# Kernel tuning notes

Measured on AMD Instinct MI355X. Metric: run time of the kernel, lower is better.

Reference implementation:

```python
import jax, jax.numpy as jnp
import numpy as np

B, T, I, H, O = 64, 256, 256, 1024, 256


def _lstm_cell(x, h, c, W_ih, W_hh, b_ih, b_hh):
    # PyTorch LSTMCell: gates = x@W_ih^T + b_ih + h@W_hh^T + b_hh, chunked as i,f,g,o
    gates = x @ W_ih.T + h @ W_hh.T + (b_ih + b_hh)
    i_g, f_g, g_g, o_g = jnp.split(gates, 4, axis=-1)
    c_new = jax.nn.sigmoid(f_g) * c + jax.nn.sigmoid(i_g) * jnp.tanh(g_g)
    h_new = jax.nn.sigmoid(o_g) * jnp.tanh(c_new)
    return h_new, c_new


def setup_inputs() -> dict:
    key = jax.random.key(0)
    ks = jax.random.split(key, 11)
    s1 = 1.0 / np.sqrt(H)
    return {
        "x": jax.random.normal(ks[0], (B, T, I), dtype=jnp.float32),
        "W_ih1": jax.random.uniform(ks[1], (4 * H, I), jnp.float32, -s1, s1),
        "W_hh1": jax.random.uniform(ks[2], (4 * H, H), jnp.float32, -s1, s1),
        "b_ih1": jax.random.uniform(ks[3], (4 * H,), jnp.float32, -s1, s1),
        "b_hh1": jax.random.uniform(ks[4], (4 * H,), jnp.float32, -s1, s1),
        "W_ih2": jax.random.uniform(ks[5], (4 * H, I + H), jnp.float32, -s1, s1),
        "W_hh2": jax.random.uniform(ks[6], (4 * H, H), jnp.float32, -s1, s1),
        "b_ih2": jax.random.uniform(ks[7], (4 * H,), jnp.float32, -s1, s1),
        "b_hh2": jax.random.uniform(ks[8], (4 * H,), jnp.float32, -s1, s1),
        "W_l": jax.random.uniform(ks[9], (O, I + H), jnp.float32, -s1, s1),
        "b_l": jax.random.uniform(ks[10], (O,), jnp.float32, -s1, s1),
    }


def reference(x, W_ih1, W_hh1, b_ih1, b_hh1, W_ih2, W_hh2, b_ih2, b_hh2, W_l, b_l):
    batch = x.shape[0]
    zeros = jnp.zeros((batch, H), dtype=x.dtype)
    init = (zeros, zeros, zeros, zeros)  # h1, c1, h2, c2

    def step(carry, x_t):
        h1, c1, h2, c2 = carry
        h1, c1 = _lstm_cell(x_t, h1, c1, W_ih1, W_hh1, b_ih1, b_hh1)
        x2 = jnp.concatenate([x_t, h1], axis=1)  # [B, I+H]
        h2, c2 = _lstm_cell(x2, h2, c2, W_ih2, W_hh2, b_ih2, b_hh2)
        x3 = jnp.concatenate([x_t, h2], axis=1)  # [B, I+H]
        y_t = x3 @ W_l.T + b_l  # [B, O]
        return (h1, c1, h2, c2), y_t

    xs = jnp.swapaxes(x, 0, 1)  # [T, B, I]
    _, ys = jax.lax.scan(step, init, xs)  # ys: [T, B, O]
    return jnp.swapaxes(ys, 0, 1)  # [B, T, O]
```

## Files before the change

kernel.cpp:

```cpp
#include <hip/hip_runtime.h>


typedef __attribute__((ext_vector_type(8))) short short8;
typedef __attribute__((ext_vector_type(16))) float f32x16;
typedef __attribute__((ext_vector_type(4))) float f32x4;

#define Tn 256
#define In 256
#define Hn 1024
#define On 256
#define SP 136
#define NL1 64
#define NL2 128
#define NY  16
#define NBLK (NL1 + NL2 + NY)
#define CHUNK_B 17408
#define SMEM_SZ 55808
#define BHe 65536
#define RELEASE_IDX 240

#define WS_WIH1 0
#define WS_WHH1 2097152
#define WS_WIH2 10485760
#define WS_WHH2 20971520
#define WS_WL   29360128
#define WS_X    30015488
#define WS_H1   38404096
#define WS_H2   38666240
#define WS_ARR  38928384

#define WAIT_LGKM0() __builtin_amdgcn_s_waitcnt(0xC07F)
#define RAW_BARRIER() do { \
    WAIT_LGKM0(); \
    __builtin_amdgcn_sched_barrier(0); \
    __builtin_amdgcn_s_barrier(); \
    __builtin_amdgcn_sched_barrier(0); \
  } while (0)

#define STAGE_WAIT(rem) do { \
    __builtin_amdgcn_sched_barrier(0); \
    if ((rem) >= 3)      asm volatile("s_waitcnt vmcnt(12)" ::: "memory"); \
    else if ((rem) == 2) asm volatile("s_waitcnt vmcnt(8)"  ::: "memory"); \
    else if ((rem) == 1) asm volatile("s_waitcnt vmcnt(4)"  ::: "memory"); \
    else                 asm volatile("s_waitcnt vmcnt(0)"  ::: "memory"); \
    __builtin_amdgcn_sched_barrier(0); \
  } while (0)

#define GLD16(dst, ptr) \
  asm volatile("global_load_dwordx4 %0, %1, off" : "=v"(dst) : "v"(ptr))
#define GLD16C(dst, ptr) \
  asm volatile("global_load_dwordx4 %0, %1, off sc1" : "=v"(dst) : "v"(ptr))

static __device__ __forceinline__ unsigned short f2b(float f) {
  union { float f; unsigned int i; } v; v.f = f;
  unsigned int u = v.i;
  return (unsigned short)((u + 0x7FFFu + ((u >> 16) & 1u)) >> 16);
}
static __device__ __forceinline__ float sigm(float x) { return 1.0f / (1.0f + __expf(-x)); }
static __device__ __forceinline__ float tanhf_(float x) {
  float ax = fabsf(x);
  float e = __expf(-2.0f * ax);
  return copysignf((1.0f - e) / (1.0f + e), x);
}
static __device__ __forceinline__ int ld32a(const void* p) {
  return __hip_atomic_load((const int*)p, __ATOMIC_RELAXED, __HIP_MEMORY_SCOPE_AGENT);
}
static __device__ __forceinline__ void st32a(void* p, unsigned int v) {
  __hip_atomic_store((unsigned int*)p, v, __ATOMIC_RELAXED, __HIP_MEMORY_SCOPE_AGENT);
}
static __device__ __forceinline__ void st64a(void* p, unsigned long long v) {
  __hip_atomic_store((unsigned long long*)p, v, __ATOMIC_RELAXED, __HIP_MEMORY_SCOPE_AGENT);
}

static __device__ __forceinline__ void grid_barrier(int* arrive, int bid, int tid,
                                                    int lane, int tgt) {
  __syncthreads();
  if (tid == 0)
    st32a(&arrive[bid], (unsigned int)tgt);
  if (bid == 0) {
    if (tid < 64) {
      bool done = false;
      while (!done) {
        bool ok = true;
        #pragma unroll
        for (int j = 0; j < 4; ++j) {
          int idx = lane + j * 64;
          if (idx < NBLK) {
            int v = ld32a(&arrive[idx]);
            ok = ok && (v >= tgt);
          }
        }
        done = __all(ok);
        if (!done) __builtin_amdgcn_s_sleep(1);
      }
      if (tid == 0)
        st32a(&arrive[RELEASE_IDX], (unsigned int)tgt);
    }
    __syncthreads();
  } else {
    if (tid == 0) {
      while (ld32a(&arrive[RELEASE_IDX]) < tgt) __builtin_amdgcn_s_sleep(1);
    }
    __syncthreads();
  }
}

__global__ void __launch_bounds__(256) cvt_bf16(const float* __restrict__ src,
                                                unsigned short* __restrict__ dst, int n4) {
  int i = blockIdx.x * blockDim.x + threadIdx.x;
  if (i >= n4) return;
  float4 v = ((const float4*)src)[i];
  ushort4 o;
  o.x = f2b(v.x); o.y = f2b(v.y); o.z = f2b(v.z); o.w = f2b(v.w);
  ((ushort4*)dst)[i] = o;
}

__global__ void __launch_bounds__(256) prep_zero(unsigned short* h1buf,
                                                 unsigned short* h2buf,
                                                 int* arrive) {
  int i = blockIdx.x * blockDim.x + threadIdx.x;
  st64a((unsigned long long*)h1buf + i, 0ull);
  st64a((unsigned long long*)h1buf + 16384 + i, 0ull);
  st64a((unsigned long long*)h2buf + i, 0ull);
  st64a((unsigned long long*)h2buf + 16384 + i, 0ull);
  if (i < 256) st32a(arrive + i, 0u);
}

__global__ void __launch_bounds__(256, 1) lstm_persist(
    const unsigned short* __restrict__ x,
    const unsigned short* __restrict__ Wih1, const unsigned short* __restrict__ Whh1,
    const float* __restrict__ bih1, const float* __restrict__ bhh1,
    const unsigned short* __restrict__ Wih2, const unsigned short* __restrict__ Whh2,
    const float* __restrict__ bih2, const float* __restrict__ bhh2,
    const unsigned short* __restrict__ Wl,  const float* __restrict__ bl,
    float* __restrict__ out,
    unsigned short* __restrict__ h1buf, unsigned short* __restrict__ h2buf,
    int* __restrict__ arrive)
{
  extern __shared__ char smem[];
  unsigned short* sbuf0 = (unsigned short*)smem;
  unsigned short* sbuf1 = (unsigned short*)(smem + CHUNK_B);
  float* sG = (float*)(smem + 2 * CHUNK_B);
  float* sc = (float*)(smem + 2 * CHUNK_B + 16896);

  const int tid = threadIdx.x;
  const int bid = blockIdx.x;
  const int lane = tid & 63;
  const int wid = tid >> 6;
  const int r0  = tid >> 4;
  const int sg  = tid & 15;

  for (int e = tid; e < 1024; e += 256) sc[e] = 0.0f;

  uint4 rs[4][4];

  if (bid < NL1) {
    const int j0 = bid << 4;
    const int mtile = wid & 1, ntile = wid >> 1;
    const int arow = mtile * 32 + (lane & 31);
    const int brow = ntile * 32 + (lane & 31);
    const int gr = ((brow >> 4) << 10) + j0 + (brow & 15);
    const int hi8 = (lane >> 5) << 3;

    short8 w[80];
    #pragma unroll
    for (int c = 0; c < 10; ++c) {
      const unsigned short* wrow = (c < 2) ? (Wih1 + (size_t)gr * In + c * 128)
                                           : (Whh1 + (size_t)gr * Hn + (c - 2) * 128);
      #pragma unroll
      for (int k8 = 0; k8 < 8; ++k8)
        w[c * 8 + k8] = *(const short8*)(wrow + k8 * 16 + hi8);
    }
    float bs[2][2][4];
    #pragma unroll
    for (int p = 0; p < 2; ++p) {
      int pi = tid + p * 256, op = (pi & 7) << 1;
      #pragma unroll
      for (int k = 0; k < 2; ++k) {
        int o = op + k;
        #pragma unroll
        for (int g = 0; g < 4; ++g)
          bs[p][k][g] = bih1[g * 1024 + j0 + o] + bhh1[g * 1024 + j0 + o];
      }
    }

    for (int s = 0; s < Tn; ++s) {
      const int t = s;
      const unsigned short* h1rd = h1buf + ((t + 1) & 1) * BHe;
      unsigned short* h1wr = h1buf + (t & 1) * BHe;
      f32x16 acc0 = {}, acc1 = {};

      auto ldc = [&](int cc, int d) {
        if (cc < 2) {
          const char* p = (const char*)(x + ((size_t)r0 * Tn + t) * In + cc * 128 + sg * 8);
          #pragma unroll
          for (int j = 0; j < 4; ++j) GLD16(rs[d][j], p + (size_t)j * (16 * Tn * In * 2));
        } else {
          const char* p = (const char*)(h1rd + (size_t)r0 * Hn + (cc - 2) * 128 + sg * 8);
          #pragma unroll
          for (int j = 0; j < 4; ++j) GLD16C(rs[d][j], p + j * (16 * Hn * 2));
        }
      };
      ldc(0, 0); ldc(1, 1); ldc(2, 2); ldc(3, 3);

      #pragma unroll
      for (int c = 0; c < 10; ++c) {
        unsigned short* buf = (c & 1) ? sbuf1 : sbuf0;
        STAGE_WAIT(9 - c);
        {
          unsigned short* db = buf + r0 * SP + sg * 8;
          #pragma unroll
          for (int j = 0; j < 4; ++j) *(uint4*)(db + j * (16 * SP)) = rs[c & 3][j];
        }
        if (c + 4 < 10) ldc(c + 4, c & 3);
        RAW_BARRIER();
        const unsigned short* ab = buf + arow * SP + hi8;
        #pragma unroll
        for (int k8 = 0; k8 < 8; k8 += 2) {
          acc0 = __builtin_amdgcn_mfma_f32_32x32x16_bf16(*(const short8*)(ab + k8 * 16),      w[c * 8 + k8],     acc0, 0, 0, 0);
          acc1 = __builtin_amdgcn_mfma_f32_32x32x16_bf16(*(const short8*)(ab + k8 * 16 + 16), w[c * 8 + k8 + 1], acc1, 0, 0, 0);
        }
      }
      RAW_BARRIER();

      f32x16 accv = acc0 + acc1;
      #pragma unroll
      for (int i = 0; i < 16; ++i) {
        int rm = (i & 3) + ((i >> 2) << 3) + ((lane >> 5) << 2);
        sG[(mtile * 32 + rm) * 65 + brow] = accv[i];
      }
      __syncthreads();

      #pragma unroll
      for (int p = 0; p < 2; ++p) {
        int pi = tid + p * 256;
        int b = pi >> 3, op = (pi & 7) << 1;
        const float* gb = sG + b * 65;
        unsigned int pack = 0;
        #pragma unroll
        for (int k = 0; k < 2; ++k) {
          int o = op + k, e = b * 16 + o;
          float ig = gb[o]      + bs[p][k][0];
          float fg = gb[16 + o] + bs[p][k][1];
          float gg = gb[32 + o] + bs[p][k][2];
          float og = gb[48 + o] + bs[p][k][3];
          float cn = sigm(fg) * sc[e] + sigm(ig) * tanhf_(gg);
          sc[e] = cn;
          pack |= ((unsigned int)f2b(sigm(og) * tanhf_(cn))) << (16 * k);
        }
        st32a(h1wr + b * Hn + j0 + op, pack);
      }
      grid_barrier(arrive, bid, tid, lane, s + 1);
    }
    grid_barrier(arrive, bid, tid, lane, Tn + 1);

  } else if (bid < NL1 + NL2) {
    const int j0 = (bid - NL1) << 3;
    const int mtile = wid & 1, ks = wid >> 1;
    const int arow = mtile * 32 + (lane & 31);
    const int brow = lane & 31;
    const int gr = ((brow >> 3) << 10) + j0 + (brow & 7);
    const int hi8 = (lane >> 5) << 3;

    short8 w[80];
    if (ks == 0) {
      #pragma unroll
      for (int c = 0; c < 10; ++c)
        #pragma unroll
        for (int k8 = 0; k8 < 8; ++k8)
          w[c * 8 + k8] = *(const short8*)(Wih2 + (size_t)gr * 1280 + c * 128 + k8 * 16 + hi8);
    } else {
      #pragma unroll
      for (int c = 0; c < 8; ++c)
        #pragma unroll
        for (int k8 = 0; k8 < 8; ++k8)
          w[c * 8 + k8] = *(const short8*)(Whh2 + (size_t)gr * Hn + c * 128 + k8 * 16 + hi8);
    }
    float bs[2][4];
    {
      int op = (tid & 3) << 1;
      #pragma unroll
      for (int k = 0; k < 2; ++k) {
        int o = op + k;
        #pragma unroll
        for (int g = 0; g < 4; ++g)
          bs[k][g] = bih2[g * 1024 + j0 + o] + bhh2[g * 1024 + j0 + o];
      }
    }

    grid_barrier(arrive, bid, tid, lane, 1);

    for (int s = 1; s <= Tn; ++s) {
      const int t = s - 1;
      const unsigned short* h1rd = h1buf + (t & 1) * BHe;
      const unsigned short* h2rd = h2buf + ((t + 1) & 1) * BHe;
      unsigned short* h2wr = h2buf + (t & 1) * BHe;
      f32x16 acc0 = {}, acc1 = {};

      auto ldc = [&](int cc, int d) {
        if (cc < 2) {
          const char* p = (const char*)(x + ((size_t)r0 * Tn + t) * In + cc * 128 + sg * 8);
          #pragma unroll
          for (int j = 0; j < 4; ++j) GLD16(rs[d][j], p + (size_t)j * (16 * Tn * In * 2));
        } else {
          const unsigned short* src = (cc < 10) ? (h1rd + (cc - 2) * 128)
                                                : (h2rd + (cc - 10) * 128);
          const char* p = (const char*)(src + (size_t)r0 * Hn + sg * 8);
          #pragma unroll
          for (int j = 0; j < 4; ++j) GLD16C(rs[d][j], p + j * (16 * Hn * 2));
        }
      };
      ldc(0, 0); ldc(1, 1); ldc(2, 2); ldc(3, 3);

      #pragma unroll
      for (int c = 0; c < 18; ++c) {
        unsigned short* buf = (c & 1) ? sbuf1 : sbuf0;
        STAGE_WAIT(17 - c);
        {
          unsigned short* db = buf + r0 * SP + sg * 8;
          #pragma unroll
          for (int j = 0; j < 4; ++j) *(uint4*)(db + j * (16 * SP)) = rs[c & 3][j];
        }
        if (c + 4 < 18) ldc(c + 4, c & 3);
        RAW_BARRIER();
        bool active = (ks == 0) ? (c < 10) : (c >= 10);
        if (active) {
          int ib = ((ks == 0) ? c : (c - 10)) * 8;
          const unsigned short* ab = buf + arow * SP + hi8;
          #pragma unroll
          for (int k8 = 0; k8 < 8; k8 += 2) {
            acc0 = __builtin_amdgcn_mfma_f32_32x32x16_bf16(*(const short8*)(ab + k8 * 16),      w[ib + k8],     acc0, 0, 0, 0);
            acc1 = __builtin_amdgcn_mfma_f32_32x32x16_bf16(*(const short8*)(ab + k8 * 16 + 16), w[ib + k8 + 1], acc1, 0, 0, 0);
          }
        }
      }
      RAW_BARRIER();

      f32x16 accv = acc0 + acc1;
      #pragma unroll
      for (int i = 0; i < 16; ++i) {
        int rm = (i & 3) + ((i >> 2) << 3) + ((lane >> 5) << 2);
        sG[ks * 2112 + (mtile * 32 + rm) * 33 + brow] = accv[i];
      }
      __syncthreads();

      {
        int b = tid >> 2, op = (tid & 3) << 1;
        const float* g0 = sG + b * 33;
        const float* g1 = sG + 2112 + b * 33;
        unsigned int pack = 0;
        #pragma unroll
        for (int k = 0; k < 2; ++k) {
          int o = op + k, e = b * 8 + o;
          float ig = g0[o]      + g1[o]      + bs[k][0];
          float fg = g0[8 + o]  + g1[8 + o]  + bs[k][1];
          float gg = g0[16 + o] + g1[16 + o] + bs[k][2];
          float og = g0[24 + o] + g1[24 + o] + bs[k][3];
          float cn = sigm(fg) * sc[e] + sigm(ig) * tanhf_(gg);
          sc[e] = cn;
          pack |= ((unsigned int)f2b(sigm(og) * tanhf_(cn))) << (16 * k);
        }
        st32a(h2wr + b * Hn + j0 + op, pack);
      }
      grid_barrier(arrive, bid, tid, lane, s + 1);
    }

  } else {
    const int o0 = (bid - NL1 - NL2) << 4;
    const int quad = lane >> 4;
    const int l15 = lane & 15;
    const int hi8y = quad << 3;

    short8 wy[40];
    #pragma unroll
    for (int c = 0; c < 10; ++c)
      #pragma unroll
      for (int q = 0; q < 4; ++q)
        wy[c * 4 + q] = *(const short8*)(Wl + (size_t)(o0 + l15) * 1280 + c * 128 + q * 32 + hi8y);
    const float blv = bl[o0 + l15];

    grid_barrier(arrive, bid, tid, lane, 1);
    grid_barrier(arrive, bid, tid, lane, 2);

    for (int s = 2; s <= Tn + 1; ++s) {
      const int t = s - 2;
      const unsigned short* h2rd = h2buf + (t & 1) * BHe;
      f32x4 acc0 = {}, acc1 = {};

      auto ldc = [&](int cc, int d) {
        if (cc < 2) {
          const char* p = (const char*)(x + ((size_t)r0 * Tn + t) * In + cc * 128 + sg * 8);
          #pragma unroll
          for (int j = 0; j < 4; ++j) GLD16(rs[d][j], p + (size_t)j * (16 * Tn * In * 2));
        } else {
          const char* p = (const char*)(h2rd + (size_t)r0 * Hn + (cc - 2) * 128 + sg * 8);
          #pragma unroll
          for (int j = 0; j < 4; ++j) GLD16C(rs[d][j], p + j * (16 * Hn * 2));
        }
      };
      ldc(0, 0); ldc(1, 1); ldc(2, 2); ldc(3, 3);

      #pragma unroll
      for (int c = 0; c < 10; ++c) {
        unsigned short* buf = (c & 1) ? sbuf1 : sbuf0;
        STAGE_WAIT(9 - c);
        {
          unsigned short* db = buf + r0 * SP + sg * 8;
          #pragma unroll
          for (int j = 0; j < 4; ++j) *(uint4*)(db + j * (16 * SP)) = rs[c & 3][j];
        }
        if (c + 4 < 10) ldc(c + 4, c & 3);
        RAW_BARRIER();
        const unsigned short* ab = buf + (wid * 16 + l15) * SP + hi8y;
        acc0 = __builtin_amdgcn_mfma_f32_16x16x32_bf16(*(const short8*)(ab),      wy[c * 4 + 0], acc0, 0, 0, 0);
        acc1 = __builtin_amdgcn_mfma_f32_16x16x32_bf16(*(const short8*)(ab + 32), wy[c * 4 + 1], acc1, 0, 0, 0);
        acc0 = __builtin_amdgcn_mfma_f32_16x16x32_bf16(*(const short8*)(ab + 64), wy[c * 4 + 2], acc0, 0, 0, 0);
        acc1 = __builtin_amdgcn_mfma_f32_16x16x32_bf16(*(const short8*)(ab + 96), wy[c * 4 + 3], acc1, 0, 0, 0);
      }
      RAW_BARRIER();

      f32x4 accv = acc0 + acc1;
      #pragma unroll
      for (int i = 0; i < 4; ++i) {
        int b = wid * 16 + quad * 4 + i;
        out[((size_t)b * Tn + t) * On + o0 + l15] = accv[i] + blv;
      }
      if (s <= Tn) grid_barrier(arrive, bid, tid, lane, s + 1);
    }
  }
}

extern "C" void kernel_launch(void* const* d_in, const int* in_sizes, int n_in,
                              void* d_out, int out_size, void* d_ws, size_t ws_size,
                              hipStream_t stream) {
  (void)in_sizes; (void)n_in; (void)out_size; (void)ws_size;
  const float* xf    = (const float*)d_in[0];
  const float* Wih1f = (const float*)d_in[1];
  const float* Whh1f = (const float*)d_in[2];
  const float* bih1  = (const float*)d_in[3];
  const float* bhh1  = (const float*)d_in[4];
  const float* Wih2f = (const float*)d_in[5];
  const float* Whh2f = (const float*)d_in[6];
  const float* bih2  = (const float*)d_in[7];
  const float* bhh2  = (const float*)d_in[8];
  const float* Wlf   = (const float*)d_in[9];
  const float* bl    = (const float*)d_in[10];
  float* out = (float*)d_out;

  char* ws = (char*)d_ws;
  unsigned short* Wih1b = (unsigned short*)(ws + WS_WIH1);
  unsigned short* Whh1b = (unsigned short*)(ws + WS_WHH1);
  unsigned short* Wih2b = (unsigned short*)(ws + WS_WIH2);
  unsigned short* Whh2b = (unsigned short*)(ws + WS_WHH2);
  unsigned short* Wlb   = (unsigned short*)(ws + WS_WL);
  unsigned short* xb    = (unsigned short*)(ws + WS_X);
  unsigned short* h1buf = (unsigned short*)(ws + WS_H1);
  unsigned short* h2buf = (unsigned short*)(ws + WS_H2);
  int* arrive           = (int*)(ws + WS_ARR);

  hipLaunchKernelGGL(cvt_bf16, dim3(1024), dim3(256), 0, stream, Wih1f, Wih1b, 262144);
  hipLaunchKernelGGL(cvt_bf16, dim3(4096), dim3(256), 0, stream, Whh1f, Whh1b, 1048576);
  hipLaunchKernelGGL(cvt_bf16, dim3(5120), dim3(256), 0, stream, Wih2f, Wih2b, 1310720);
  hipLaunchKernelGGL(cvt_bf16, dim3(4096), dim3(256), 0, stream, Whh2f, Whh2b, 1048576);
  hipLaunchKernelGGL(cvt_bf16, dim3(320),  dim3(256), 0, stream, Wlf,   Wlb,   81920);
  hipLaunchKernelGGL(cvt_bf16, dim3(4096), dim3(256), 0, stream, xf,    xb,    1048576);

  hipLaunchKernelGGL(prep_zero, dim3(64), dim3(256), 0, stream, h1buf, h2buf, arrive);

  hipLaunchKernelGGL(lstm_persist, dim3(NBLK), dim3(256), SMEM_SZ, stream,
                     xb, Wih1b, Whh1b, bih1, bhh1, Wih2b, Whh2b, bih2, bhh2, Wlb, bl,
                     out, h1buf, h2buf, arrive);
}
```

Before: 2.349 ms.

## Split LSTM layer blocks across batch halves and widen hidden tiles per block

Layer-1 and layer-2 blocks now each handle half of the batch (32 rows) but a wider slice of hidden units: 32 units per layer-1 block and 16 per layer-2 block. Each block therefore loads half as much activation data per step from global memory, with a shallower vmcnt wait schedule. Layer-2 rebalances its split-K work between the two wave groups to 9 chunks each instead of 10 and 8. The per-block weight register footprint stays about the same, while the block count and the grid-barrier participants are unchanged. Gate layouts in LDS and the h-store widths are rewritten to match the new tiling.

```diff
diff --git a/kernel.cpp b/kernel.cpp
--- a/kernel.cpp
+++ b/kernel.cpp
@@ -37,7 +37,16 @@
     __builtin_amdgcn_sched_barrier(0); \
   } while (0)
 
-#define STAGE_WAIT(rem) do { \
+#define STAGE_WAIT2(rem) do { \
+    __builtin_amdgcn_sched_barrier(0); \
+    if ((rem) >= 3)      asm volatile("s_waitcnt vmcnt(6)" ::: "memory"); \
+    else if ((rem) == 2) asm volatile("s_waitcnt vmcnt(4)" ::: "memory"); \
+    else if ((rem) == 1) asm volatile("s_waitcnt vmcnt(2)" ::: "memory"); \
+    else                 asm volatile("s_waitcnt vmcnt(0)" ::: "memory"); \
+    __builtin_amdgcn_sched_barrier(0); \
+  } while (0)
+
+#define STAGE_WAIT4(rem) do { \
     __builtin_amdgcn_sched_barrier(0); \
     if ((rem) >= 3)      asm volatile("s_waitcnt vmcnt(12)" ::: "memory"); \
     else if ((rem) == 2) asm volatile("s_waitcnt vmcnt(8)"  ::: "memory"); \
@@ -149,18 +158,18 @@
   const int wid = tid >> 6;
   const int r0  = tid >> 4;
   const int sg  = tid & 15;
+  const int l31 = lane & 31;
+  const int hi8 = (lane >> 5) << 3;
 
   for (int e = tid; e < 1024; e += 256) sc[e] = 0.0f;
 
-  uint4 rs[4][4];
-
   if (bid < NL1) {
-    const int j0 = bid << 4;
-    const int mtile = wid & 1, ntile = wid >> 1;
-    const int arow = mtile * 32 + (lane & 31);
-    const int brow = ntile * 32 + (lane & 31);
-    const int gr = ((brow >> 4) << 10) + j0 + (brow & 15);
-    const int hi8 = (lane >> 5) << 3;
+    const int bh = bid & 1;
+    const int rb = bh << 5;
+    const int j0 = (bid >> 1) << 5;
+    const int gr = wid * 1024 + j0 + l31;
+
+    uint4 rs[4][2];
 
     short8 w[80];
     #pragma unroll
@@ -171,16 +180,15 @@
       for (int k8 = 0; k8 < 8; ++k8)
         w[c * 8 + k8] = *(const short8*)(wrow + k8 * 16 + hi8);
     }
-    float bs[2][2][4];
-    #pragma unroll
-    for (int p = 0; p < 2; ++p) {
-      int pi = tid + p * 256, op = (pi & 7) << 1;
-      #pragma unroll
-      for (int k = 0; k < 2; ++k) {
-        int o = op + k;
+    float bs[4][4];
+    {
+      int op4 = (tid & 7) << 2;
+      #pragma unroll
+      for (int k = 0; k < 4; ++k) {
+        int o = op4 + k;
         #pragma unroll
         for (int g = 0; g < 4; ++g)
-          bs[p][k][g] = bih1[g * 1024 + j0 + o] + bhh1[g * 1024 + j0 + o];
+          bs[k][g] = bih1[g * 1024 + j0 + o] + bhh1[g * 1024 + j0 + o];
       }
     }
 
@@ -192,13 +200,13 @@
 
       auto ldc = [&](int cc, int d) {
         if (cc < 2) {
-          const char* p = (const char*)(x + ((size_t)r0 * Tn + t) * In + cc * 128 + sg * 8);
-          #pragma unroll
-          for (int j = 0; j < 4; ++j) GLD16(rs[d][j], p + (size_t)j * (16 * Tn * In * 2));
+          const char* p = (const char*)(x + ((size_t)(rb + r0) * Tn + t) * In + cc * 128 + sg * 8);
+          GLD16(rs[d][0], p);
+          GLD16(rs[d][1], p + 16 * Tn * In * 2);
         } else {
-          const char* p = (const char*)(h1rd + (size_t)r0 * Hn + (cc - 2) * 128 + sg * 8);
-          #pragma unroll
-          for (int j = 0; j < 4; ++j) GLD16C(rs[d][j], p + j * (16 * Hn * 2));
+          const char* p = (const char*)(h1rd + (size_t)(rb + r0) * Hn + (cc - 2) * 128 + sg * 8);
+          GLD16C(rs[d][0], p);
+          GLD16C(rs[d][1], p + 16 * Hn * 2);
         }
       };
       ldc(0, 0); ldc(1, 1); ldc(2, 2); ldc(3, 3);
@@ -206,15 +214,15 @@
       #pragma unroll
       for (int c = 0; c < 10; ++c) {
         unsigned short* buf = (c & 1) ? sbuf1 : sbuf0;
-        STAGE_WAIT(9 - c);
+        STAGE_WAIT2(9 - c);
         {
           unsigned short* db = buf + r0 * SP + sg * 8;
-          #pragma unroll
-          for (int j = 0; j < 4; ++j) *(uint4*)(db + j * (16 * SP)) = rs[c & 3][j];
+          *(uint4*)db = rs[c & 3][0];
+          *(uint4*)(db + 16 * SP) = rs[c & 3][1];
         }
         if (c + 4 < 10) ldc(c + 4, c & 3);
         RAW_BARRIER();
-        const unsigned short* ab = buf + arow * SP + hi8;
+        const unsigned short* ab = buf + l31 * SP + hi8;
         #pragma unroll
         for (int k8 = 0; k8 < 8; k8 += 2) {
           acc0 = __builtin_amdgcn_mfma_f32_32x32x16_bf16(*(const short8*)(ab + k8 * 16),      w[c * 8 + k8],     acc0, 0, 0, 0);
@@ -227,61 +235,66 @@
       #pragma unroll
       for (int i = 0; i < 16; ++i) {
         int rm = (i & 3) + ((i >> 2) << 3) + ((lane >> 5) << 2);
-        sG[(mtile * 32 + rm) * 65 + brow] = accv[i];
+        sG[wid * 1056 + rm * 33 + l31] = accv[i];
       }
       __syncthreads();
 
-      #pragma unroll
-      for (int p = 0; p < 2; ++p) {
-        int pi = tid + p * 256;
-        int b = pi >> 3, op = (pi & 7) << 1;
-        const float* gb = sG + b * 65;
-        unsigned int pack = 0;
-        #pragma unroll
-        for (int k = 0; k < 2; ++k) {
-          int o = op + k, e = b * 16 + o;
-          float ig = gb[o]      + bs[p][k][0];
-          float fg = gb[16 + o] + bs[p][k][1];
-          float gg = gb[32 + o] + bs[p][k][2];
-          float og = gb[48 + o] + bs[p][k][3];
+      {
+        int b = tid >> 3, op4 = (tid & 7) << 2;
+        unsigned int pk0 = 0, pk1 = 0;
+        #pragma unroll
+        for (int k = 0; k < 4; ++k) {
+          int o = op4 + k, e = b * 32 + o;
+          float ig = sG[       b * 33 + o] + bs[k][0];
+          float fg = sG[1056 + b * 33 + o] + bs[k][1];
+          float gg = sG[2112 + b * 33 + o] + bs[k][2];
+          float og = sG[3168 + b * 33 + o] + bs[k][3];
           float cn = sigm(fg) * sc[e] + sigm(ig) * tanhf_(gg);
           sc[e] = cn;
-          pack |= ((unsigned int)f2b(sigm(og) * tanhf_(cn))) << (16 * k);
-        }
-        st32a(h1wr + b * Hn + j0 + op, pack);
+          unsigned int hb = f2b(sigm(og) * tanhf_(cn));
+          if (k < 2) pk0 |= hb << (16 * k); else pk1 |= hb << (16 * (k - 2));
+        }
+        st64a(h1wr + (size_t)(rb + b) * Hn + j0 + op4,
+              ((unsigned long long)pk1 << 32) | pk0);
       }
       grid_barrier(arrive, bid, tid, lane, s + 1);
     }
     grid_barrier(arrive, bid, tid, lane, Tn + 1);
 
   } else if (bid < NL1 + NL2) {
-    const int j0 = (bid - NL1) << 3;
-    const int mtile = wid & 1, ks = wid >> 1;
-    const int arow = mtile * 32 + (lane & 31);
-    const int brow = lane & 31;
-    const int gr = ((brow >> 3) << 10) + j0 + (brow & 7);
-    const int hi8 = (lane >> 5) << 3;
-
-    short8 w[80];
+    const int lb = bid - NL1;
+    const int bh = lb & 1;
+    const int rb = bh << 5;
+    const int j0 = (lb >> 1) << 4;
+    const int ntile = wid & 1, ks = wid >> 1;
+    const int grow = ntile * 32 + l31;
+    const int gr = ((grow >> 4) << 10) + j0 + (grow & 15);
+
+    uint4 rs[4][2];
+
+    short8 w[72];
     if (ks == 0) {
       #pragma unroll
-      for (int c = 0; c < 10; ++c)
+      for (int c = 0; c < 9; ++c)
         #pragma unroll
         for (int k8 = 0; k8 < 8; ++k8)
           w[c * 8 + k8] = *(const short8*)(Wih2 + (size_t)gr * 1280 + c * 128 + k8 * 16 + hi8);
     } else {
       #pragma unroll
-      for (int c = 0; c < 8; ++c)
+      for (int c = 0; c < 9; ++c) {
+        const unsigned short* wrow = (c == 0) ? (Wih2 + (size_t)gr * 1280 + 1152)
+                                              : (Whh2 + (size_t)gr * Hn + (c - 1) * 128);
         #pragma unroll
         for (int k8 = 0; k8 < 8; ++k8)
-          w[c * 8 + k8] = *(const short8*)(Whh2 + (size_t)gr * Hn + c * 128 + k8 * 16 + hi8);
+          w[c * 8 + k8] = *(const short8*)(wrow + k8 * 16 + hi8);
+      }
     }
     float bs[2][4];
     {
-      int op = (tid & 3) << 1;
+      int op2 = (tid & 7) << 1;
       #pragma unroll
       for (int k = 0; k < 2; ++k) {
-        int o = op + k;
+        int o = op2 + k;
         #pragma unroll
         for (int g = 0; g < 4; ++g)
           bs[k][g] = bih2[g * 1024 + j0 + o] + bhh2[g * 1024 + j0 + o];
@@ -299,15 +312,15 @@
 
       auto ldc = [&](int cc, int d) {
         if (cc < 2) {
-          const char* p = (const char*)(x + ((size_t)r0 * Tn + t) * In + cc * 128 + sg * 8);
-          #pragma unroll
-          for (int j = 0; j < 4; ++j) GLD16(rs[d][j], p + (size_t)j * (16 * Tn * In * 2));
+          const char* p = (const char*)(x + ((size_t)(rb + r0) * Tn + t) * In + cc * 128 + sg * 8);
+          GLD16(rs[d][0], p);
+          GLD16(rs[d][1], p + 16 * Tn * In * 2);
         } else {
           const unsigned short* src = (cc < 10) ? (h1rd + (cc - 2) * 128)
                                                 : (h2rd + (cc - 10) * 128);
-          const char* p = (const char*)(src + (size_t)r0 * Hn + sg * 8);
-          #pragma unroll
-          for (int j = 0; j < 4; ++j) GLD16C(rs[d][j], p + j * (16 * Hn * 2));
+          const char* p = (const char*)(src + (size_t)(rb + r0) * Hn + sg * 8);
+          GLD16C(rs[d][0], p);
+          GLD16C(rs[d][1], p + 16 * Hn * 2);
         }
       };
       ldc(0, 0); ldc(1, 1); ldc(2, 2); ldc(3, 3);
@@ -315,18 +328,18 @@
       #pragma unroll
       for (int c = 0; c < 18; ++c) {
         unsigned short* buf = (c & 1) ? sbuf1 : sbuf0;
-        STAGE_WAIT(17 - c);
+        STAGE_WAIT2(17 - c);
         {
           unsigned short* db = buf + r0 * SP + sg * 8;
-          #pragma unroll
-          for (int j = 0; j < 4; ++j) *(uint4*)(db + j * (16 * SP)) = rs[c & 3][j];
+          *(uint4*)db = rs[c & 3][0];
+          *(uint4*)(db + 16 * SP) = rs[c & 3][1];
         }
         if (c + 4 < 18) ldc(c + 4, c & 3);
         RAW_BARRIER();
-        bool active = (ks == 0) ? (c < 10) : (c >= 10);
+        bool active = (ks == 0) ? (c < 9) : (c >= 9);
         if (active) {
-          int ib = ((ks == 0) ? c : (c - 10)) * 8;
-          const unsigned short* ab = buf + arow * SP + hi8;
+          int ib = ((ks == 0) ? c : (c - 9)) * 8;
+          const unsigned short* ab = buf + l31 * SP + hi8;
           #pragma unroll
           for (int k8 = 0; k8 < 8; k8 += 2) {
             acc0 = __builtin_amdgcn_mfma_f32_32x32x16_bf16(*(const short8*)(ab + k8 * 16),      w[ib + k8],     acc0, 0, 0, 0);
@@ -340,27 +353,25 @@
       #pragma unroll
       for (int i = 0; i < 16; ++i) {
         int rm = (i & 3) + ((i >> 2) << 3) + ((lane >> 5) << 2);
-        sG[ks * 2112 + (mtile * 32 + rm) * 33 + brow] = accv[i];
+        sG[ks * 2112 + grow * 33 + rm] = accv[i];
       }
       __syncthreads();
 
       {
-        int b = tid >> 2, op = (tid & 3) << 1;
-        const float* g0 = sG + b * 33;
-        const float* g1 = sG + 2112 + b * 33;
+        int b = tid >> 3, op2 = (tid & 7) << 1;
         unsigned int pack = 0;
         #pragma unroll
         for (int k = 0; k < 2; ++k) {
-          int o = op + k, e = b * 8 + o;
-          float ig = g0[o]      + g1[o]      + bs[k][0];
-          float fg = g0[8 + o]  + g1[8 + o]  + bs[k][1];
-          float gg = g0[16 + o] + g1[16 + o] + bs[k][2];
-          float og = g0[24 + o] + g1[24 + o] + bs[k][3];
+          int o = op2 + k, e = b * 16 + o;
+          float ig = sG[(     o) * 33 + b] + sG[2112 + (     o) * 33 + b] + bs[k][0];
+          float fg = sG[(16 + o) * 33 + b] + sG[2112 + (16 + o) * 33 + b] + bs[k][1];
+          float gg = sG[(32 + o) * 33 + b] + sG[2112 + (32 + o) * 33 + b] + bs[k][2];
+          float og = sG[(48 + o) * 33 + b] + sG[2112 + (48 + o) * 33 + b] + bs[k][3];
           float cn = sigm(fg) * sc[e] + sigm(ig) * tanhf_(gg);
           sc[e] = cn;
           pack |= ((unsigned int)f2b(sigm(og) * tanhf_(cn))) << (16 * k);
         }
-        st32a(h2wr + b * Hn + j0 + op, pack);
+        st32a(h2wr + (size_t)(rb + b) * Hn + j0 + op2, pack);
       }
       grid_barrier(arrive, bid, tid, lane, s + 1);
     }
@@ -370,6 +381,8 @@
     const int quad = lane >> 4;
     const int l15 = lane & 15;
     const int hi8y = quad << 3;
+
+    uint4 rs[4][4];
 
     short8 wy[40];
     #pragma unroll
@@ -403,7 +416,7 @@
       #pragma unroll
       for (int c = 0; c < 10; ++c) {
         unsigned short* buf = (c & 1) ? sbuf1 : sbuf0;
-        STAGE_WAIT(9 - c);
+        STAGE_WAIT4(9 - c);
         {
           unsigned short* db = buf + r0 * SP + sg * 8;
           #pragma unroll
```

Result: faster. 2.150 ms (-8.5%).
